# Kernel optimization log

Measured on AMD Instinct MI355X. Metric: run time of the kernel, lower is better.

Reference implementation:

```python
import math
import jax, jax.numpy as jnp
import numpy as np

B, T, C = 8, 1024, 768
H = 12
D = C // H  # 64


def setup_inputs() -> dict:
    key = jax.random.key(0)
    k1, k2, k3, k4, k5 = jax.random.split(key, 5)
    s = 0.02
    return {
        "x": jax.random.normal(k1, (B, T, C), dtype=jnp.float32),
        "w_qkv": jax.random.normal(k2, (C, 3 * C), dtype=jnp.float32) * s,
        "b_qkv": jax.random.normal(k3, (3 * C,), dtype=jnp.float32) * s,
        "w_proj": jax.random.normal(k4, (C, C), dtype=jnp.float32) * s,
        "b_proj": jax.random.normal(k5, (C,), dtype=jnp.float32) * s,
    }


def reference(x, w_qkv, b_qkv, w_proj, b_proj):
    b, t, c = x.shape
    qkv = x @ w_qkv + b_qkv                      # [B,T,3C]
    q, k, v = jnp.split(qkv, 3, axis=-1)
    # [B,T,C] -> [B,H,T,D]
    q = q.reshape(b, t, H, D).transpose(0, 2, 1, 3)
    k = k.reshape(b, t, H, D).transpose(0, 2, 1, 3)
    v = v.reshape(b, t, H, D).transpose(0, 2, 1, 3)
    scale = 1.0 / math.sqrt(D)
    att = jnp.einsum("bhqd,bhkd->bhqk", q, k) * scale   # [B,H,T,T]
    causal = jnp.tril(jnp.ones((t, t), dtype=bool))
    att = jnp.where(causal, att, -jnp.inf)
    att = jax.nn.softmax(att, axis=-1)
    y = jnp.einsum("bhqk,bhkd->bhqd", att, v)            # [B,H,T,D]
    y = y.transpose(0, 2, 1, 3).reshape(b, t, c)
    return y @ w_proj + b_proj
```

## Files before the change

### kernel.cpp

```cpp
#include <hip/hip_runtime.h>
#include <math.h>

#define B_ 8
#define T_ 1024
#define C_ 768
#define H_ 12
#define D_ 64

typedef __bf16 bf16x8 __attribute__((ext_vector_type(8)));
typedef float  f32x4  __attribute__((ext_vector_type(4)));
typedef unsigned short us8 __attribute__((ext_vector_type(8)));
typedef unsigned int   u32x4v __attribute__((ext_vector_type(4)));

typedef __attribute__((address_space(3))) void lds_void;
typedef __attribute__((address_space(1))) const void glb_void;

#define KSC 0.18033688011112043f

__device__ __forceinline__ unsigned short f2bf(float f) {
    unsigned int u = __float_as_uint(f);
    u += 0x7fffu + ((u >> 16) & 1u);
    return (unsigned short)(u >> 16);
}

__global__ __launch_bounds__(256)
void prep_w(const float* __restrict__ x,
            const float* __restrict__ w_qkv, const float* __restrict__ b_qkv,
            const float* __restrict__ w_proj,
            unsigned short* __restrict__ wqT, unsigned short* __restrict__ wpT,
            float* __restrict__ bqs, unsigned short* __restrict__ xb) {
    __shared__ unsigned short Ts[64][65];
    const int id  = blockIdx.x;
    const int tid = threadIdx.x;
    if (id >= 577) {
        const int xid = id - 577;
        const float4* xi = (const float4*)x;
        ushort4* xo = (ushort4*)xb;
#pragma unroll
        for (int it = 0; it < 6; it++) {
            const int idx = (xid * 6 + it) * 256 + tid;
            float4 v = xi[idx];
            ushort4 o;
            o.x = f2bf(v.x); o.y = f2bf(v.y); o.z = f2bf(v.z); o.w = f2bf(v.w);
            xo[idx] = o;
        }
        return;
    }
    if (id == 576) {
        for (int i = tid; i < 3 * C_; i += 256)
            bqs[i] = b_qkv[i] * (i < C_ ? KSC : 1.f);
        return;
    }
    const float* W; unsigned short* Wt; int N, nlim, t2;
    if (id < 432) { t2 = id;       W = w_qkv;  Wt = wqT; N = 3 * C_; nlim = C_; }
    else          { t2 = id - 432; W = w_proj; Wt = wpT; N = C_;     nlim = 0;  }
    const int ntiles = N / 64;
    const int n0 = (t2 % ntiles) * 64, k0 = (t2 / ntiles) * 64;
    for (int i = tid; i < 4096; i += 256) {
        int n = i & 63, k = i >> 6;
        float sc = (n0 + n < nlim) ? KSC : 1.f;
        Ts[n][k] = f2bf(W[(size_t)(k0 + k) * N + n0 + n] * sc);
    }
    __syncthreads();
    for (int i = tid; i < 4096; i += 256) {
        int k = i & 63, n = i >> 6;
        Wt[(size_t)(n0 + n) * 768 + k0 + k] = Ts[n][k];
    }
}

template<int OUT_BF16>
__global__ __launch_bounds__(256, 2)
void gemm_pipe(const unsigned short* __restrict__ A16,
               const unsigned short* __restrict__ Bt, const float* __restrict__ bias,
               void* __restrict__ Cout, int M, int N, int K) {
    __shared__ __align__(16) unsigned short As[2][8192];
    __shared__ __align__(16) unsigned short Bs[2][8192];

    const int tid  = threadIdx.x;
    const int lane = tid & 63;
    const int c    = lane & 15;
    const int quad = lane >> 4;
    const int wave = tid >> 6;
    const int wm   = (wave >> 1) * 64;
    const int wn   = (wave & 1) * 64;
    const int bm   = blockIdx.x * 128;
    const int bn   = blockIdx.y * 128;

    const unsigned short* aS[4];
    const unsigned short* bS[4];
#pragma unroll
    for (int p = 0; p < 4; p++) {
        const int Lp = p * 256 + tid;
        const int L  = Lp ^ ((Lp >> 3) & 7);
        aS[p] = A16 + (size_t)(bm + (L >> 3)) * K + (L & 7) * 8;
        bS[p] = Bt  + (size_t)(bn + (L >> 3)) * K + (L & 7) * 8;
    }
    const int wb = (tid & 0xC0) * 8;

    int aoff[4][2], boff[4][2];
#pragma unroll
    for (int i = 0; i < 4; i++)
#pragma unroll
        for (int ks = 0; ks < 2; ks++) {
            const int kcA = (ks * 4 + quad) ^ (c & 7);
            aoff[i][ks] = ((wm + i * 16 + c) * 8 + kcA) * 8;
            boff[i][ks] = ((wn + i * 16 + c) * 8 + kcA) * 8;
        }

    f32x4 acc[4][4];
#pragma unroll
    for (int i = 0; i < 4; i++)
#pragma unroll
        for (int j = 0; j < 4; j++) acc[i][j] = (f32x4){0.f, 0.f, 0.f, 0.f};

#pragma unroll
    for (int p = 0; p < 4; p++) {
        __builtin_amdgcn_global_load_lds((glb_void*)aS[p],
            (lds_void*)(&As[0][0] + p * 2048 + wb), 16, 0, 0);
        aS[p] += 64;
        __builtin_amdgcn_global_load_lds((glb_void*)bS[p],
            (lds_void*)(&Bs[0][0] + p * 2048 + wb), 16, 0, 0);
        bS[p] += 64;
    }

    const int R = K >> 6;
    for (int r = 0; r < R; r++) {
        __syncthreads();

        if (r + 1 < R) {
#pragma unroll
            for (int p = 0; p < 4; p++) {
                __builtin_amdgcn_global_load_lds((glb_void*)aS[p],
                    (lds_void*)(&As[(r + 1) & 1][0] + p * 2048 + wb), 16, 0, 0);
                aS[p] += 64;
                __builtin_amdgcn_global_load_lds((glb_void*)bS[p],
                    (lds_void*)(&Bs[(r + 1) & 1][0] + p * 2048 + wb), 16, 0, 0);
                bS[p] += 64;
            }
        }

        const unsigned short* abuf = &As[r & 1][0];
        const unsigned short* bbuf = &Bs[r & 1][0];
#pragma unroll
        for (int ks = 0; ks < 2; ks++) {
            bf16x8 af[4], bfr[4];
#pragma unroll
            for (int i = 0; i < 4; i++)
                af[i] = __builtin_bit_cast(bf16x8, *(const us8*)&abuf[aoff[i][ks]]);
#pragma unroll
            for (int j = 0; j < 4; j++)
                bfr[j] = __builtin_bit_cast(bf16x8, *(const us8*)&bbuf[boff[j][ks]]);
#pragma unroll
            for (int i = 0; i < 4; i++)
#pragma unroll
                for (int j = 0; j < 4; j++)
                    acc[i][j] = __builtin_amdgcn_mfma_f32_16x16x32_bf16(af[i], bfr[j], acc[i][j], 0, 0, 0);
        }
    }

    float bs[4];
#pragma unroll
    for (int j = 0; j < 4; j++) bs[j] = bias[bn + wn + j * 16 + c];
#pragma unroll
    for (int i = 0; i < 4; i++) {
        const int gm = bm + wm + i * 16 + quad * 4;
#pragma unroll
        for (int r = 0; r < 4; r++) {
            const size_t ro = (size_t)(gm + r) * N;
#pragma unroll
            for (int j = 0; j < 4; j++) {
                const float v = acc[i][j][r] + bs[j];
                const int gn = bn + wn + j * 16 + c;
                if (OUT_BF16) ((unsigned short*)Cout)[ro + gn] = f2bf(v);
                else          ((float*)Cout)[ro + gn] = v;
            }
        }
    }
}

__device__ __forceinline__ int sigmaK(int k) {
    return 16 * (2 * (k >> 5) + ((k >> 2) & 1)) + 4 * ((k >> 3) & 3) + (k & 3);
}

__global__ __launch_bounds__(256, 3)
void attn_mfma(const unsigned short* __restrict__ qkv, unsigned short* __restrict__ y) {
    __shared__ __align__(16) unsigned short Ks[64 * 72];
    __shared__ __align__(16) unsigned int   Vt[64 * 36];

    const int tid  = threadIdx.x;
    const int wave = tid >> 6;
    const int lane = tid & 63;
    const int c    = lane & 15;
    const int quad = lane >> 4;

    const int id = blockIdx.x;
    const int p  = (id >> 3) & 7;
    const int bh = (id >> 6) * 8 + (id & 7);
    const int b  = bh / H_;
    const int h  = bh - b * H_;

    const int qts[2] = {p, 15 - p};
    const int q0s[2] = {p * 64, (15 - p) * 64};

    const int RS = 3 * C_;
    const unsigned short* kbase = qkv + (size_t)b * T_ * RS + C_ + h * D_;
    const unsigned short* vbase = qkv + (size_t)b * T_ * RS + 2 * C_ + h * D_;

    const u32x4v onesu = {0x3F803F80u, 0x3F803F80u, 0x3F803F80u, 0x3F803F80u};
    const bf16x8 onesf = __builtin_bit_cast(bf16x8, onesu);

    bf16x8 qf[2][2];
#pragma unroll
    for (int t = 0; t < 2; t++) {
        const unsigned short* qrow =
            qkv + ((size_t)(b * T_ + q0s[t] + wave * 16 + c)) * RS + h * D_ + quad * 8;
        qf[t][0] = __builtin_bit_cast(bf16x8, *(const us8*)qrow);
        qf[t][1] = __builtin_bit_cast(bf16x8, *(const us8*)(qrow + 32));
    }

    const int kr0 = tid >> 3, kc0 = tid & 7;
    const int sK0 = sigmaK(kr0) * 72 + kc0 * 8;
    const int sK1 = sigmaK(kr0 + 32) * 72 + kc0 * 8;
    const int dg  = tid >> 4, kp0 = tid & 15;

    us8 kA, kB;
    ushort4 vA0, vB0, vA1, vB1;
    {
        kA = *(const us8*)(kbase + (size_t)kr0 * RS + kc0 * 8);
        kB = *(const us8*)(kbase + (size_t)(kr0 + 32) * RS + kc0 * 8);
        const unsigned short* p0 = vbase + (size_t)(2 * kp0) * RS + dg * 4;
        vA0 = *(const ushort4*)p0;  vB0 = *(const ushort4*)(p0 + RS);
        const unsigned short* p1 = vbase + (size_t)(2 * (kp0 + 16)) * RS + dg * 4;
        vA1 = *(const ushort4*)p1;  vB1 = *(const ushort4*)(p1 + RS);
    }

    f32x4 Oa[2][4];
    f32x4 Ol[2];
#pragma unroll
    for (int t = 0; t < 2; t++) {
        Ol[t] = (f32x4){0.f, 0.f, 0.f, 0.f};
#pragma unroll
        for (int d = 0; d < 4; d++) Oa[t][d] = (f32x4){0.f, 0.f, 0.f, 0.f};
    }

    const int ktEnd = qts[1];
    for (int kt = 0; kt <= ktEnd; kt++) {
        __syncthreads();
        *(us8*)&Ks[sK0] = kA;
        *(us8*)&Ks[sK1] = kB;
        {
            unsigned int* v0 = &Vt[(dg * 4) * 36 + kp0];
            v0[0]   = vA0.x | ((unsigned)vB0.x << 16);
            v0[36]  = vA0.y | ((unsigned)vB0.y << 16);
            v0[72]  = vA0.z | ((unsigned)vB0.z << 16);
            v0[108] = vA0.w | ((unsigned)vB0.w << 16);
            unsigned int* v1 = v0 + 16;
            v1[0]   = vA1.x | ((unsigned)vB1.x << 16);
            v1[36]  = vA1.y | ((unsigned)vB1.y << 16);
            v1[72]  = vA1.z | ((unsigned)vB1.z << 16);
            v1[108] = vA1.w | ((unsigned)vB1.w << 16);
        }
        __syncthreads();

        if (kt < ktEnd) {
            const unsigned short* kp = kbase + (size_t)((kt + 1) * 64) * RS;
            kA = *(const us8*)(kp + (size_t)kr0 * RS + kc0 * 8);
            kB = *(const us8*)(kp + (size_t)(kr0 + 32) * RS + kc0 * 8);
            const unsigned short* vp = vbase + (size_t)((kt + 1) * 64) * RS;
            const unsigned short* p0 = vp + (size_t)(2 * kp0) * RS + dg * 4;
            vA0 = *(const ushort4*)p0;  vB0 = *(const ushort4*)(p0 + RS);
            const unsigned short* p1 = vp + (size_t)(2 * (kp0 + 16)) * RS + dg * 4;
            vA1 = *(const ushort4*)p1;  vB1 = *(const ushort4*)(p1 + RS);
        }

        bf16x8 kf[4][2];
#pragma unroll
        for (int nb = 0; nb < 4; nb++) {
#pragma unroll
            for (int ks = 0; ks < 2; ks++)
                kf[nb][ks] = __builtin_bit_cast(bf16x8,
                    *(const us8*)&Ks[(nb * 16 + c) * 72 + quad * 8 + ks * 32]);
        }

#pragma unroll
        for (int t = 0; t < 2; t++) {
            if (kt > qts[t]) continue;
            const bool diag = (kt == qts[t]);
            const bool doHi = !diag || (wave >= 2);
            const int nbmax = diag ? ((wave >= 2) ? 3 : 1) : 3;

            f32x4 sv[4];
#pragma unroll
            for (int nb = 0; nb < 4; nb++) {
                if (nb <= nbmax) {
                    f32x4 z = (f32x4){0.f, 0.f, 0.f, 0.f};
                    z = __builtin_amdgcn_mfma_f32_16x16x32_bf16(kf[nb][0], qf[t][0], z, 0, 0, 0);
                    sv[nb] = __builtin_amdgcn_mfma_f32_16x16x32_bf16(kf[nb][1], qf[t][1], z, 0, 0, 0);
                }
            }
            if (diag) {
                const int qloc = wave * 16 + c;
#pragma unroll
                for (int nb = 0; nb < 4; nb++) {
                    if (nb <= nbmax) {
                        const int kb = 32 * (nb >> 1) + 4 * (nb & 1) + 8 * quad;
#pragma unroll
                        for (int r = 0; r < 4; r++)
                            if (kb + r > qloc) sv[nb][r] = -INFINITY;
                    }
                }
            }

            unsigned int pd[4][2];
#pragma unroll
            for (int nb = 0; nb < 4; nb++) {
                if (nb <= nbmax) {
                    float p0 = __builtin_amdgcn_exp2f(sv[nb][0]);
                    float p1 = __builtin_amdgcn_exp2f(sv[nb][1]);
                    float p2 = __builtin_amdgcn_exp2f(sv[nb][2]);
                    float p3 = __builtin_amdgcn_exp2f(sv[nb][3]);
                    unsigned u0 = __float_as_uint(p0) + 0x8000u;
                    unsigned u1 = __float_as_uint(p1) + 0x8000u;
                    unsigned u2 = __float_as_uint(p2) + 0x8000u;
                    unsigned u3 = __float_as_uint(p3) + 0x8000u;
                    pd[nb][0] = (u0 >> 16) | (u1 & 0xffff0000u);
                    pd[nb][1] = (u2 >> 16) | (u3 & 0xffff0000u);
                } else {
                    pd[nb][0] = 0u; pd[nb][1] = 0u;
                }
            }

            bf16x8 ap0 = __builtin_bit_cast(bf16x8,
                (u32x4v){pd[0][0], pd[0][1], pd[1][0], pd[1][1]});
            bf16x8 ap1 = __builtin_bit_cast(bf16x8,
                (u32x4v){pd[2][0], pd[2][1], pd[3][0], pd[3][1]});

            Ol[t] = __builtin_amdgcn_mfma_f32_16x16x32_bf16(ap0, onesf, Ol[t], 0, 0, 0);
            if (doHi)
                Ol[t] = __builtin_amdgcn_mfma_f32_16x16x32_bf16(ap1, onesf, Ol[t], 0, 0, 0);

#pragma unroll
            for (int dd = 0; dd < 4; dd++) {
                const unsigned int* vrow = &Vt[(dd * 16 + c) * 36 + quad * 4];
                bf16x8 vb0 = __builtin_bit_cast(bf16x8, *(const u32x4v*)vrow);
                Oa[t][dd] = __builtin_amdgcn_mfma_f32_16x16x32_bf16(ap0, vb0, Oa[t][dd], 0, 0, 0);
                if (doHi) {
                    bf16x8 vb1 = __builtin_bit_cast(bf16x8, *(const u32x4v*)(vrow + 16));
                    Oa[t][dd] = __builtin_amdgcn_mfma_f32_16x16x32_bf16(ap1, vb1, Oa[t][dd], 0, 0, 0);
                }
            }
        }
    }

#pragma unroll
    for (int t = 0; t < 2; t++) {
        unsigned short* yrow =
            y + ((size_t)(b * T_ + q0s[t] + wave * 16)) * C_ + h * D_;
#pragma unroll
        for (int r = 0; r < 4; r++) {
            float inv = 1.f / Ol[t][r];
#pragma unroll
            for (int dd = 0; dd < 4; dd++)
                yrow[(size_t)(quad * 4 + r) * C_ + dd * 16 + c] = f2bf(Oa[t][dd][r] * inv);
        }
    }
}

extern "C" void kernel_launch(void* const* d_in, const int* in_sizes, int n_in,
                              void* d_out, int out_size, void* d_ws, size_t ws_size,
                              hipStream_t stream) {
    const float* x      = (const float*)d_in[0];
    const float* w_qkv  = (const float*)d_in[1];
    const float* b_qkv  = (const float*)d_in[2];
    const float* w_proj = (const float*)d_in[3];
    const float* b_proj = (const float*)d_in[4];
    float* out = (float*)d_out;

    unsigned short* wqT  = (unsigned short*)d_ws;
    unsigned short* wpT  = wqT  + (size_t)3 * C_ * C_;
    unsigned short* qkvb = wpT  + (size_t)C_ * C_;
    unsigned short* yb   = qkvb + (size_t)B_ * T_ * 3 * C_;
    float*          bqs  = (float*)(yb + (size_t)B_ * T_ * C_);

    unsigned short* xb = yb;

    prep_w<<<1601, 256, 0, stream>>>(x, w_qkv, b_qkv, w_proj, wqT, wpT, bqs, xb);

    gemm_pipe<1><<<dim3(B_ * T_ / 128, 3 * C_ / 128), 256, 0, stream>>>(
        xb, wqT, bqs, qkvb, B_ * T_, 3 * C_, C_);

    attn_mfma<<<8 * B_ * H_, 256, 0, stream>>>(qkvb, yb);

    gemm_pipe<0><<<dim3(B_ * T_ / 128, C_ / 128), 256, 0, stream>>>(
        yb, wpT, b_proj, out, B_ * T_, C_, C_);
}
```

Before: 181.7 us.

## Add 256x256-tile 512-thread GEMM kernel for the QKV projection

Adds a new GEMM kernel with 256x256 output tiles, 8 waves per block each computing 128x64, double-buffered async global-to-LDS loads, and setprio around MFMA bursts. The QKV projection now uses it instead of the 128x128 pipelined kernel. The larger tile raises arithmetic intensity and data reuse per LDS load. The cost is fewer blocks (32x9=288), which may underfill the GPU, plus higher register and LDS use that lowers occupancy.

```diff
diff --git a/kernel.cpp b/kernel.cpp
--- a/kernel.cpp
+++ b/kernel.cpp
@@ -65,6 +65,130 @@
     for (int i = tid; i < 4096; i += 256) {
         int k = i & 63, n = i >> 6;
         Wt[(size_t)(n0 + n) * 768 + k0 + k] = Ts[n][k];
+    }
+}
+
+__global__ __launch_bounds__(512, 2)
+void gemm256(const unsigned short* __restrict__ A16,
+             const unsigned short* __restrict__ Bt, const float* __restrict__ bias,
+             unsigned short* __restrict__ Cout, int M, int N, int K) {
+    __shared__ __align__(16) unsigned short As[2][16384];
+    __shared__ __align__(16) unsigned short Bs[2][16384];
+
+    const int tid  = threadIdx.x;
+    const int lane = tid & 63;
+    const int c    = lane & 15;
+    const int quad = lane >> 4;
+    const int wave = tid >> 6;
+    const int wm   = (wave >> 2) * 128;
+    const int wn   = (wave & 3) * 64;
+    const int bm   = blockIdx.x * 256;
+    const int bn   = blockIdx.y * 256;
+
+    const unsigned short* aS[4];
+    const unsigned short* bS[4];
+#pragma unroll
+    for (int p = 0; p < 4; p++) {
+        const int Lp = p * 512 + tid;
+        const int L  = Lp ^ ((Lp >> 3) & 7);
+        aS[p] = A16 + (size_t)(bm + (L >> 3)) * K + (L & 7) * 8;
+        bS[p] = Bt  + (size_t)(bn + (L >> 3)) * K + (L & 7) * 8;
+    }
+    const int wb = (tid & 0x1C0) * 8;
+
+    int aofs[2], bofs[2];
+#pragma unroll
+    for (int ks = 0; ks < 2; ks++) {
+        const int kc = (ks * 4 + quad) ^ (c & 7);
+        aofs[ks] = (wm + c) * 64 + kc * 8;
+        bofs[ks] = (wn + c) * 64 + kc * 8;
+    }
+
+    f32x4 acc[8][4];
+#pragma unroll
+    for (int i = 0; i < 8; i++)
+#pragma unroll
+        for (int j = 0; j < 4; j++) acc[i][j] = (f32x4){0.f, 0.f, 0.f, 0.f};
+
+#pragma unroll
+    for (int p = 0; p < 4; p++) {
+        __builtin_amdgcn_global_load_lds((glb_void*)aS[p],
+            (lds_void*)(&As[0][0] + p * 4096 + wb), 16, 0, 0);
+        aS[p] += 64;
+        __builtin_amdgcn_global_load_lds((glb_void*)bS[p],
+            (lds_void*)(&Bs[0][0] + p * 4096 + wb), 16, 0, 0);
+        bS[p] += 64;
+    }
+
+    const int R = K >> 6;
+    for (int t = 0; t < R; t++) {
+        asm volatile("s_barrier" ::: "memory");
+        if (t + 1 < R) {
+#pragma unroll
+            for (int p = 0; p < 4; p++) {
+                __builtin_amdgcn_global_load_lds((glb_void*)aS[p],
+                    (lds_void*)(&As[(t + 1) & 1][0] + p * 4096 + wb), 16, 0, 0);
+                aS[p] += 64;
+                __builtin_amdgcn_global_load_lds((glb_void*)bS[p],
+                    (lds_void*)(&Bs[(t + 1) & 1][0] + p * 4096 + wb), 16, 0, 0);
+                bS[p] += 64;
+            }
+            asm volatile("s_waitcnt vmcnt(8)" ::: "memory");
+        } else {
+            asm volatile("s_waitcnt vmcnt(0)" ::: "memory");
+        }
+        asm volatile("s_barrier" ::: "memory");
+
+        const unsigned short* ab = &As[t & 1][0];
+        const unsigned short* bb = &Bs[t & 1][0];
+
+#pragma unroll
+        for (int ks = 0; ks < 2; ks++) {
+            bf16x8 bfr[4], af[4];
+#pragma unroll
+            for (int j = 0; j < 4; j++)
+                bfr[j] = __builtin_bit_cast(bf16x8, *(const us8*)&bb[bofs[ks] + j * 1024]);
+#pragma unroll
+            for (int i = 0; i < 4; i++)
+                af[i] = __builtin_bit_cast(bf16x8, *(const us8*)&ab[aofs[ks] + i * 1024]);
+            __builtin_amdgcn_s_setprio(1);
+#pragma unroll
+            for (int i = 0; i < 4; i++)
+#pragma unroll
+                for (int j = 0; j < 4; j++)
+                    acc[i][j] = __builtin_amdgcn_mfma_f32_16x16x32_bf16(af[i], bfr[j], acc[i][j], 0, 0, 0);
+            __builtin_amdgcn_s_setprio(0);
+            asm volatile("s_barrier" ::: "memory");
+#pragma unroll
+            for (int i = 0; i < 4; i++)
+                af[i] = __builtin_bit_cast(bf16x8, *(const us8*)&ab[aofs[ks] + (i + 4) * 1024]);
+            __builtin_amdgcn_s_setprio(1);
+#pragma unroll
+            for (int i = 0; i < 4; i++)
+#pragma unroll
+                for (int j = 0; j < 4; j++)
+                    acc[i + 4][j] = __builtin_amdgcn_mfma_f32_16x16x32_bf16(af[i], bfr[j], acc[i + 4][j], 0, 0, 0);
+            __builtin_amdgcn_s_setprio(0);
+            if (ks == 0)
+                asm volatile("s_barrier" ::: "memory");
+        }
+    }
+
+    float bsv[4];
+#pragma unroll
+    for (int j = 0; j < 4; j++) bsv[j] = bias[bn + wn + j * 16 + c];
+#pragma unroll
+    for (int i = 0; i < 8; i++) {
+        const int gm = bm + wm + i * 16 + quad * 4;
+#pragma unroll
+        for (int r = 0; r < 4; r++) {
+            const size_t ro = (size_t)(gm + r) * N;
+#pragma unroll
+            for (int j = 0; j < 4; j++) {
+                const float v = acc[i][j][r] + bsv[j];
+                Cout[ro + bn + wn + j * 16 + c] = f2bf(v);
+            }
+        }
     }
 }
 
@@ -386,7 +510,7 @@
 
     prep_w<<<1601, 256, 0, stream>>>(x, w_qkv, b_qkv, w_proj, wqT, wpT, bqs, xb);
 
-    gemm_pipe<1><<<dim3(B_ * T_ / 128, 3 * C_ / 128), 256, 0, stream>>>(
+    gemm256<<<dim3(B_ * T_ / 256, 3 * C_ / 256), 512, 0, stream>>>(
         xb, wqT, bqs, qkvb, B_ * T_, 3 * C_, C_);
 
     attn_mfma<<<8 * B_ * H_, 256, 0, stream>>>(qkvb, yb);
```

After: 196.0 us. +7.9%, slower.
